# Performance work log

Measured on AMD Instinct MI355X. Metric: run time of the kernel, lower is better.

Reference implementation:

```python
import jax, jax.numpy as jnp
import numpy as np

DIM = 512
HEADS = 16
HEAD_DIM = DIM // HEADS
WH, WW = 7, 7
N = WH * WW
OUP = 512
SCALE = HEAD_DIM ** -0.5
NW = 64  # windows per image (mask leading dim)


def _relative_position_index():
    coords = np.stack(np.meshgrid(np.arange(WH), np.arange(WW), indexing='ij'))  # (2,Wh,Ww)
    flat = coords.reshape(2, -1)                           # (2, N)
    rel = flat[:, :, None] - flat[:, None, :]              # (2, N, N)
    rel = rel.transpose(1, 2, 0).astype(np.int64)          # (N, N, 2)
    rel[:, :, 0] += WH - 1
    rel[:, :, 1] += WW - 1
    rel[:, :, 0] *= 2 * WW - 1
    return jnp.asarray(rel.sum(-1))                        # (N, N) int

REL_IDX = _relative_position_index()


def setup_inputs() -> dict:
    key = jax.random.key(0)
    ks = jax.random.split(key, 8)
    B_ = 4096
    x = jax.random.normal(ks[0], (B_, N, DIM), dtype=jnp.float32)
    mask = jnp.zeros((NW, N, N), dtype=jnp.float32)
    qkv_w = jax.random.normal(ks[1], (3 * DIM, DIM), dtype=jnp.float32) * (DIM ** -0.5)
    qkv_b = jax.random.normal(ks[2], (3 * DIM,), dtype=jnp.float32) * 0.02
    table = jax.random.normal(ks[3], ((2 * WH - 1) * (2 * WW - 1), HEADS), dtype=jnp.float32) * 0.02
    proj_w = jax.random.normal(ks[4], (OUP, DIM), dtype=jnp.float32) * (DIM ** -0.5)
    proj_b = jax.random.normal(ks[5], (OUP,), dtype=jnp.float32) * 0.02
    return {"x": x, "mask": mask, "qkv_w": qkv_w, "qkv_b": qkv_b,
            "table": table, "proj_w": proj_w, "proj_b": proj_b}


def reference(x, mask, qkv_w, qkv_b, table, proj_w, proj_b):
    B_, n, c = x.shape
    qkv = x @ qkv_w.T + qkv_b                               # (B_, N, 3C)
    qkv = qkv.reshape(B_, n, 3, HEADS, HEAD_DIM).transpose(2, 0, 3, 1, 4)
    q, k, v = qkv[0], qkv[1], qkv[2]                        # (B_, H, N, hd)
    q = q * SCALE
    attn = jnp.einsum('bhnd,bhmd->bhnm', q, k)              # (B_, H, N, N)
    bias = table[REL_IDX]                                   # (N, N, H) gather
    attn = attn + bias.transpose(2, 0, 1)[None]             # add rel-pos bias
    nW = mask.shape[0]
    attn = attn.reshape(B_ // nW, nW, HEADS, n, n) + mask[None, :, None]
    attn = attn.reshape(B_, HEADS, n, n)
    attn = jax.nn.softmax(attn, axis=-1)
    out = jnp.einsum('bhnm,bhmd->bhnd', attn, v)            # (B_, H, N, hd)
    out = out.transpose(0, 2, 1, 3).reshape(B_, n, c)
    return out @ proj_w.T + proj_b
```

## Files before the change

### kernel.cpp

```cpp
#include <hip/hip_runtime.h>
#include <hip/hip_bf16.h>
#include <stdint.h>

#define DIMC 512
#define HEADS 16
#define HEAD_DIM 32
#define NTOK 49
#define SCALE 0.17677669529663687f

typedef unsigned short u16;
typedef short bf16x8 __attribute__((ext_vector_type(8)));
typedef float f32x4 __attribute__((ext_vector_type(4)));
typedef u16 u16x4 __attribute__((ext_vector_type(4)));
typedef u16 u16x8 __attribute__((ext_vector_type(8)));

#define MFMA16(a, b, c) __builtin_amdgcn_mfma_f32_16x16x32_bf16((a), (b), (c), 0, 0, 0)

__device__ __forceinline__ u16 f2bf(float f) {
  __hip_bfloat16 h = __float2bfloat16(f);
  u16 u;
  __builtin_memcpy(&u, &h, 2);
  return u;
}

__device__ __forceinline__ float bf2f(u16 u) {
  const uint32_t b = ((uint32_t)u) << 16;
  float f;
  __builtin_memcpy(&f, &b, 4);
  return f;
}

__device__ __forceinline__ void gld16(const void* g, void* l) {
  __builtin_amdgcn_global_load_lds(
      (const __attribute__((address_space(1))) uint32_t*)g,
      (__attribute__((address_space(3))) uint32_t*)l, 16, 0, 0);
}

__global__ void cvt_f32_bf16(const float* __restrict__ in, u16* __restrict__ out, int n) {
  const int stride = gridDim.x * blockDim.x;
  for (int i = blockIdx.x * blockDim.x + threadIdx.x; i * 8 < n; i += stride) {
    const float4 v0 = ((const float4*)(in + i * 8))[0];
    const float4 v1 = ((const float4*)(in + i * 8))[1];
    u16x8 r;
    r[0] = f2bf(v0.x); r[1] = f2bf(v0.y); r[2] = f2bf(v0.z); r[3] = f2bf(v0.w);
    r[4] = f2bf(v1.x); r[5] = f2bf(v1.y); r[6] = f2bf(v1.z); r[7] = f2bf(v1.w);
    *(u16x8*)(out + i * 8) = r;
  }
}

__global__ void biasmask_kernel(const float* __restrict__ table, const float* __restrict__ mask,
                                u16* __restrict__ bm) {
  const int wm = blockIdx.x >> 4;
  const int h  = blockIdx.x & 15;
  for (int e = threadIdx.x; e < 4096; e += 256) {
    const int r = e & 3, lane = (e >> 2) & 63, fj = (e >> 8) & 3, fi = e >> 10;
    const int row = fi * 16 + (lane >> 4) * 4 + r;
    const int col = fj * 16 + (lane & 15);
    float v;
    if (row < NTOK && col < NTOK) {
      const int yi = row / 7, xi = row % 7, yj = col / 7, xj = col % 7;
      const int idx = (yi - yj + 6) * 13 + (xi - xj + 6);
      v = table[idx * HEADS + h] + mask[wm * (NTOK * NTOK) + row * NTOK + col];
    } else {
      v = -1e30f;
    }
    bm[(size_t)blockIdx.x * 4096 + e] = f2bf(v);
  }
}

template<bool OUT_BF16, bool QKV_SCALE>
__global__ void gemm_bf16(const u16* __restrict__ Ap, const u16* __restrict__ Bp,
                          const float* __restrict__ bias, void* __restrict__ Cp,
                          int M, int N, int K, int nxt) {
  __shared__ u16 As[128 * 64];
  __shared__ u16 Bs[128 * 64];
  const int t = threadIdx.x;
  const int lane = t & 63;
  const int q = gridDim.x >> 3;
  const int lin = blockIdx.x;
  const int l = (lin & 7) * q + (lin >> 3);
  const int bm0 = (l / nxt) * 128;
  const int bn0 = (l % nxt) * 128;
  const int wv = t >> 6, wr = wv >> 1, wc = wv & 1;
  const int lr = lane & 15, lg = lane >> 4;

  f32x4 acc[4][4] = {};

  int soff[4];
#pragma unroll
  for (int k = 0; k < 4; ++k) {
    const int c = t + 256 * k;
    const int row = c >> 3, sub = c & 7;
    soff[k] = ((sub ^ (row & 7)) * 8);
  }

  const int nK = K >> 6;
  for (int kt = 0; kt < nK; ++kt) {
    const int k0 = kt << 6;
    __syncthreads();
#pragma unroll
    for (int k = 0; k < 4; ++k) {
      const int c = t + 256 * k;
      const int row = c >> 3;
      gld16(Ap + (size_t)(bm0 + row) * K + k0 + soff[k], As + c * 8);
      gld16(Bp + (size_t)(bn0 + row) * K + k0 + soff[k], Bs + c * 8);
    }
    __syncthreads();

#pragma unroll
    for (int kk = 0; kk < 2; ++kk) {
      bf16x8 af[4], bfr[4];
#pragma unroll
      for (int i = 0; i < 4; ++i) {
        const int row = wr * 64 + i * 16 + lr;
        af[i] = *(const bf16x8*)&As[row * 64 + (((kk * 4 + lg) ^ (row & 7)) << 3)];
      }
#pragma unroll
      for (int j = 0; j < 4; ++j) {
        const int row = wc * 64 + j * 16 + lr;
        bfr[j] = *(const bf16x8*)&Bs[row * 64 + (((kk * 4 + lg) ^ (row & 7)) << 3)];
      }
#pragma unroll
      for (int i = 0; i < 4; ++i)
#pragma unroll
        for (int j = 0; j < 4; ++j)
          acc[i][j] = MFMA16(af[i], bfr[j], acc[i][j]);
    }
  }

#pragma unroll
  for (int j = 0; j < 4; ++j) {
    const int col = bn0 + wc * 64 + j * 16 + lr;
    const float bv = bias[col];
    const float sc = (QKV_SCALE && col < DIMC) ? SCALE : 1.0f;
#pragma unroll
    for (int i = 0; i < 4; ++i) {
      const int row0 = bm0 + wr * 64 + i * 16 + lg * 4;
#pragma unroll
      for (int r = 0; r < 4; ++r) {
        const float val = (acc[i][j][r] + bv) * sc;
        if (OUT_BF16)
          ((u16*)Cp)[(size_t)(row0 + r) * N + col] = f2bf(val);
        else
          ((float*)Cp)[(size_t)(row0 + r) * N + col] = val;
      }
    }
  }
}

__global__ void attn_win(const u16* __restrict__ qkv, const u16* __restrict__ bmfrag,
                         u16* __restrict__ aout) {
  __shared__ u16 P[4][64 * 64];
  __shared__ u16 Vs[4][64 * 40];
  const int t = threadIdx.x, lane = t & 63, wv = t >> 6;
  const int lr = lane & 15, lg = lane >> 4;
  const int w = blockIdx.x >> 2;
  const int h = ((blockIdx.x & 3) << 2) + wv;
  const size_t base = (size_t)w * NTOK * 1536 + h * HEAD_DIM;

  const u16* bmp = bmfrag + (((size_t)(w & 63) * 16 + h) << 12);
  f32x4 s[4][4];
#pragma unroll
  for (int i = 0; i < 4; ++i)
#pragma unroll
    for (int j = 0; j < 4; ++j) {
      const u16x4 b4 = *(const u16x4*)&bmp[((i * 4 + j) * 64 + lane) * 4];
#pragma unroll
      for (int r = 0; r < 4; ++r) s[i][j][r] = bf2f(b4[r]);
    }

  const bf16x8 zf = {};
  bf16x8 qf[4], kf[4];
#pragma unroll
  for (int i = 0; i < 4; ++i) {
    const int row = i * 16 + lr;
    const size_t roff = base + (size_t)row * 1536 + lg * 8;
    qf[i] = (row < NTOK) ? *(const bf16x8*)&qkv[roff] : zf;
    kf[i] = (row < NTOK) ? *(const bf16x8*)&qkv[roff + DIMC] : zf;
  }

  u16x8 vreg[4];
  const u16x8 vz = {};
#pragma unroll
  for (int it = 0; it < 4; ++it) {
    const int k = it * 16 + (lane >> 2);
    const int seg = lane & 3;
    vreg[it] = (k < NTOK) ? *(const u16x8*)&qkv[base + 2 * DIMC + (size_t)k * 1536 + seg * 8]
                          : vz;
  }

  __builtin_amdgcn_s_setprio(1);
#pragma unroll
  for (int i = 0; i < 4; ++i)
#pragma unroll
    for (int j = 0; j < 4; ++j)
      s[i][j] = MFMA16(qf[i], kf[j], s[i][j]);
  __builtin_amdgcn_s_setprio(0);

  u16* Vsw = &Vs[wv][0];
#pragma unroll
  for (int it = 0; it < 4; ++it) {
    const int k = it * 16 + (lane >> 2);
    const int seg = lane & 3;
    *(u16x8*)&Vsw[k * 40 + seg * 8] = vreg[it];
  }

  u16* Pw = &P[wv][0];
#pragma unroll
  for (int i = 0; i < 4; ++i)
#pragma unroll
    for (int r = 0; r < 4; ++r) {
      const int ii = i * 16 + lg * 4 + r;
#pragma unroll
      for (int j = 0; j < 4; ++j) {
        const int jj = j * 16 + lr;
        Pw[ii * 64 + (((jj >> 3) ^ (ii & 7)) << 3) + (jj & 7)] = f2bf(__expf(s[i][j][r]));
      }
    }

  bf16x8 ones;
#pragma unroll
  for (int e = 0; e < 8; ++e) ones[e] = (short)0x3F80;
  f32x4 o[4][2] = {};
  f32x4 osum[4] = {};
#pragma unroll
  for (int ks = 0; ks < 2; ++ks) {
    bf16x8 vf[2];
#pragma unroll
    for (int dn = 0; dn < 2; ++dn) {
#pragma unroll
      for (int e = 0; e < 8; ++e) {
        const int kk = ks * 32 + lg * 8 + e;
        vf[dn][e] = (short)Vsw[kk * 40 + dn * 16 + lr];
      }
    }
    __builtin_amdgcn_s_setprio(1);
#pragma unroll
    for (int i = 0; i < 4; ++i) {
      const int row = i * 16 + lr;
      const bf16x8 pa = *(const bf16x8*)&Pw[row * 64 + (((ks * 4 + lg) ^ (row & 7)) << 3)];
#pragma unroll
      for (int dn = 0; dn < 2; ++dn)
        o[i][dn] = MFMA16(pa, vf[dn], o[i][dn]);
      osum[i] = MFMA16(pa, ones, osum[i]);
    }
    __builtin_amdgcn_s_setprio(0);
  }

#pragma unroll
  for (int i = 0; i < 4; ++i)
#pragma unroll
    for (int r = 0; r < 4; ++r) {
      const int row = i * 16 + lg * 4 + r;
      if (row < NTOK) {
        const float rinv = __builtin_amdgcn_rcpf(osum[i][r]);
        const size_t ob = ((size_t)w * NTOK + row) * DIMC + h * HEAD_DIM;
#pragma unroll
        for (int dn = 0; dn < 2; ++dn)
          aout[ob + dn * 16 + lr] = f2bf(o[i][dn][r] * rinv);
      }
    }
}

extern "C" void kernel_launch(void* const* d_in, const int* in_sizes, int n_in,
                              void* d_out, int out_size, void* d_ws, size_t ws_size,
                              hipStream_t stream) {
  const float* x      = (const float*)d_in[0];
  const float* mask   = (const float*)d_in[1];
  const float* qkv_w  = (const float*)d_in[2];
  const float* qkv_b  = (const float*)d_in[3];
  const float* table  = (const float*)d_in[4];
  const float* proj_w = (const float*)d_in[5];
  const float* proj_b = (const float*)d_in[6];
  float* out = (float*)d_out;

  const int M = 4096 * NTOK;

  char* ws = (char*)d_ws;
  u16*   qkv_bf   = (u16*)ws;
  u16*   wqkv_bf  = (u16*)(ws + 616562688ull);
  u16*   wproj_bf = (u16*)(ws + 618135552ull);
  u16*   biasmask = (u16*)(ws + 618659840ull);
  u16*   x_bf     = (u16*)(ws + 627048448ull);
  u16*   attn_bf  = x_bf;

  cvt_f32_bf16<<<768, 256, 0, stream>>>(qkv_w, wqkv_bf, 1536 * 512);
  cvt_f32_bf16<<<256, 256, 0, stream>>>(proj_w, wproj_bf, 512 * 512);
  biasmask_kernel<<<1024, 256, 0, stream>>>(table, mask, biasmask);
  cvt_f32_bf16<<<1792, 256, 0, stream>>>(x, x_bf, M * DIMC);

  gemm_bf16<true, true><<<1568 * 12, 256, 0, stream>>>(
      x_bf, wqkv_bf, qkv_b, qkv_bf, M, 1536, 512, 12);

  attn_win<<<4096 * 4, 256, 0, stream>>>(qkv_bf, biasmask, attn_bf);

  gemm_bf16<false, false><<<1568 * 4, 256, 0, stream>>>(
      attn_bf, wproj_bf, proj_b, out, M, 512, 512, 4);
}
```

Baseline: 1.061 ms.

## Triple-buffer GEMM shared-memory tiles with async prefetch two stages ahead

Converts the bf16 GEMM mainloop from single-buffered load-sync-compute into a 3-stage LDS ring. Global-to-LDS loads for tile kt+2 are issued before computing tile kt, with explicit vmcnt waits and raw s_barrier calls replacing __syncthreads. MFMA bursts are wrapped in s_setprio to favour math issue. LDS use triples to 96KB per block, which may reduce occupancy, and correctness now depends on the vmcnt counts matching the number of outstanding loads.

```diff
diff --git a/kernel.cpp b/kernel.cpp
--- a/kernel.cpp
+++ b/kernel.cpp
@@ -72,8 +72,8 @@
 __global__ void gemm_bf16(const u16* __restrict__ Ap, const u16* __restrict__ Bp,
                           const float* __restrict__ bias, void* __restrict__ Cp,
                           int M, int N, int K, int nxt) {
-  __shared__ u16 As[128 * 64];
-  __shared__ u16 Bs[128 * 64];
+  __shared__ u16 As[3][128 * 64];
+  __shared__ u16 Bs[3][128 * 64];
   const int t = threadIdx.x;
   const int lane = t & 63;
   const int q = gridDim.x >> 3;
@@ -86,47 +86,65 @@
 
   f32x4 acc[4][4] = {};
 
-  int soff[4];
+  int srow[4], soff[4];
 #pragma unroll
   for (int k = 0; k < 4; ++k) {
     const int c = t + 256 * k;
-    const int row = c >> 3, sub = c & 7;
-    soff[k] = ((sub ^ (row & 7)) * 8);
+    srow[k] = c >> 3;
+    soff[k] = (((c & 7) ^ (srow[k] & 7)) * 8);
   }
 
   const int nK = K >> 6;
+
+#define STAGE(KT, B)                                                            \
+  {                                                                             \
+    const int k0_ = (KT) << 6;                                                  \
+    _Pragma("unroll")                                                           \
+    for (int k = 0; k < 4; ++k) {                                               \
+      const int c = t + 256 * k;                                                \
+      gld16(Ap + (size_t)(bm0 + srow[k]) * K + k0_ + soff[k], &As[B][c * 8]);   \
+      gld16(Bp + (size_t)(bn0 + srow[k]) * K + k0_ + soff[k], &Bs[B][c * 8]);   \
+    }                                                                           \
+  }
+
+  STAGE(0, 0);
+  STAGE(1, 1);
+
   for (int kt = 0; kt < nK; ++kt) {
-    const int k0 = kt << 6;
-    __syncthreads();
-#pragma unroll
-    for (int k = 0; k < 4; ++k) {
-      const int c = t + 256 * k;
-      const int row = c >> 3;
-      gld16(Ap + (size_t)(bm0 + row) * K + k0 + soff[k], As + c * 8);
-      gld16(Bp + (size_t)(bn0 + row) * K + k0 + soff[k], Bs + c * 8);
-    }
-    __syncthreads();
-
+    if (kt + 2 < nK) STAGE(kt + 2, (kt + 2) % 3);
+    if (kt + 2 < nK)      asm volatile("s_waitcnt vmcnt(16)" ::: "memory");
+    else if (kt + 1 < nK) asm volatile("s_waitcnt vmcnt(8)" ::: "memory");
+    else                  asm volatile("s_waitcnt vmcnt(0)" ::: "memory");
+    __builtin_amdgcn_s_barrier();
+    __builtin_amdgcn_sched_barrier(0);
+
+    const u16* Asb = &As[kt % 3][0];
+    const u16* Bsb = &Bs[kt % 3][0];
 #pragma unroll
     for (int kk = 0; kk < 2; ++kk) {
       bf16x8 af[4], bfr[4];
 #pragma unroll
       for (int i = 0; i < 4; ++i) {
         const int row = wr * 64 + i * 16 + lr;
-        af[i] = *(const bf16x8*)&As[row * 64 + (((kk * 4 + lg) ^ (row & 7)) << 3)];
+        af[i] = *(const bf16x8*)&Asb[row * 64 + (((kk * 4 + lg) ^ (row & 7)) << 3)];
       }
 #pragma unroll
       for (int j = 0; j < 4; ++j) {
         const int row = wc * 64 + j * 16 + lr;
-        bfr[j] = *(const bf16x8*)&Bs[row * 64 + (((kk * 4 + lg) ^ (row & 7)) << 3)];
-      }
+        bfr[j] = *(const bf16x8*)&Bsb[row * 64 + (((kk * 4 + lg) ^ (row & 7)) << 3)];
+      }
+      __builtin_amdgcn_s_setprio(1);
 #pragma unroll
       for (int i = 0; i < 4; ++i)
 #pragma unroll
         for (int j = 0; j < 4; ++j)
           acc[i][j] = MFMA16(af[i], bfr[j], acc[i][j]);
-    }
-  }
+      __builtin_amdgcn_s_setprio(0);
+    }
+    __builtin_amdgcn_sched_barrier(0);
+    __builtin_amdgcn_s_barrier();
+  }
+#undef STAGE
 
 #pragma unroll
   for (int j = 0; j < 4; ++j) {
```

Measured after the change: 1.572 ms. 48.1% more time.
